# Performance work log

Measured on AMD Instinct MI355X. Metric: run time of the kernel, lower is better.

Reference implementation:

```python
import jax, jax.numpy as jnp
import numpy as np

B, NQ, NK = 4, 512, 512
DQ, DK, DV = 512, 512, 512
H = 128
MASK_VAL = -1e6


def setup_inputs() -> dict:
    key = jax.random.key(0)
    kq, kk, kv, kwq, kwk, kwv, kl = jax.random.split(key, 7)
    queries = jax.random.normal(kq, (B, NQ, DQ), dtype=jnp.float32)
    keys = jax.random.normal(kk, (B, NK, DK), dtype=jnp.float32)
    values = jax.random.normal(kv, (B, NK, DV), dtype=jnp.float32)
    # Dense(num_hiddens, use_bias=False) weights, Glorot-ish scale
    Wq = jax.random.normal(kwq, (DQ, H), dtype=jnp.float32) / np.sqrt(DQ)
    Wk = jax.random.normal(kwk, (DK, H), dtype=jnp.float32) / np.sqrt(DK)
    Wv = jax.random.normal(kwv, (H,), dtype=jnp.float32) / np.sqrt(H)  # Dense(1) as a vector
    valid_lens = jax.random.randint(kl, (B,), 1, NK + 1, dtype=jnp.int32)
    return {"queries": queries, "keys": keys, "values": values,
            "Wq": Wq, "Wk": Wk, "Wv": Wv, "valid_lens": valid_lens}


def reference(queries, keys, values, Wq, Wk, Wv, valid_lens):
    # Project queries/keys to hidden dim
    q = jnp.einsum('bqd,dh->bqh', queries, Wq)   # [B,NQ,H]
    k = jnp.einsum('bkd,dh->bkh', keys, Wk)      # [B,NK,H]
    # Broadcast add + tanh -> [B,NQ,NK,H] (the big intermediate)
    features = jnp.tanh(q[:, :, None, :] + k[:, None, :, :])
    # W_v reduces hidden dim to a scalar score
    scores = jnp.einsum('bqkh,h->bqk', features, Wv)  # [B,NQ,NK]
    # masked softmax over keys: positions >= valid_len get -1e6 (as in d2l sequence_mask)
    mask = jnp.arange(NK, dtype=jnp.int32)[None, None, :] < valid_lens[:, None, None]
    scores = jnp.where(mask, scores, MASK_VAL)
    attn = jax.nn.softmax(scores, axis=-1)
    # dropout rate 0.0 -> identity
    return jnp.einsum('bqk,bkv->bqv', attn, values)  # [B,NQ,DV]
```

## Files before the change

kernel.cpp:

```cpp
#include <hip/hip_runtime.h>

#ifndef __has_builtin
#define __has_builtin(x) 0
#endif

#if __has_builtin(__builtin_amdgcn_exp2f)
#define EXP2F(x) __builtin_amdgcn_exp2f(x)
#else
#define EXP2F(x) exp2f(x)
#endif
#if __has_builtin(__builtin_amdgcn_rcpf)
#define RCPF(x) __builtin_amdgcn_rcpf(x)
#else
#define RCPF(x) (1.0f / (x))
#endif

static constexpr int NB = 4, NQ = 512, NK = 512, DD = 512, HH = 128, DV = 512;
static constexpr float MASKV = -1e6f;
static constexpr float C2LOG2E = 2.885390081777926814f;

typedef __attribute__((ext_vector_type(8))) short bf16x8;
typedef __attribute__((ext_vector_type(4))) float f32x4;

__device__ __forceinline__ unsigned short f2bf(float x) {
  unsigned int u = __float_as_uint(x);
  u += 0x7FFFu + ((u >> 16) & 1u);
  return (unsigned short)(u >> 16);
}

__global__ __launch_bounds__(256) void proj_gemm_kernel(
    const float* __restrict__ queries, const float* __restrict__ keys,
    const float* __restrict__ Wq, const float* __restrict__ Wk,
    const int* __restrict__ valid_lens, float* __restrict__ projpart) {
  const int mt = blockIdx.x >> 3;
  const int ks = blockIdx.x & 7;
  const int row0 = mt << 6;
  const int k0 = ks << 6;
  const float* inb;
  const float* W;
  if (row0 >= 2048) {
    const int local = row0 - 2048;
    if ((local & 511) >= valid_lens[local >> 9]) return;
    inb = keys + (size_t)local * DD;
    W = Wk;
  } else {
    inb = queries + (size_t)row0 * DD;
    W = Wq;
  }

  __shared__ float aS[64][65];
  __shared__ __align__(16) float bS[64][128];

  const int t = threadIdx.x;
#pragma unroll
  for (int f = 0; f < 4; ++f) {
    const int idx = t + (f << 8);
    const int r = idx >> 4, d0 = (idx & 15) << 2;
    const float4 v = *reinterpret_cast<const float4*>(inb + (size_t)r * DD + k0 + d0);
    aS[r][d0] = v.x; aS[r][d0 + 1] = v.y; aS[r][d0 + 2] = v.z; aS[r][d0 + 3] = v.w;
  }
#pragma unroll
  for (int f = 0; f < 8; ++f) {
    const int idx = t + (f << 8);
    const int dk = idx >> 5, c4 = (idx & 31) << 2;
    *reinterpret_cast<float4*>(&bS[dk][c4]) =
        *reinterpret_cast<const float4*>(W + (size_t)(k0 + dk) * HH + c4);
  }
  __syncthreads();

  const int tv = t & 15, tr = t >> 4;
  float acc[4][8];
#pragma unroll
  for (int i = 0; i < 4; ++i)
#pragma unroll
    for (int j = 0; j < 8; ++j) acc[i][j] = 0.f;

#pragma unroll 8
  for (int dk = 0; dk < 64; ++dk) {
    const float av[4] = {aS[(tr << 2) + 0][dk], aS[(tr << 2) + 1][dk],
                         aS[(tr << 2) + 2][dk], aS[(tr << 2) + 3][dk]};
    const float4 b0 = *reinterpret_cast<const float4*>(&bS[dk][tv << 2]);
    const float4 b1 = *reinterpret_cast<const float4*>(&bS[dk][64 + (tv << 2)]);
    const float bv[8] = {b0.x, b0.y, b0.z, b0.w, b1.x, b1.y, b1.z, b1.w};
#pragma unroll
    for (int i = 0; i < 4; ++i)
#pragma unroll
      for (int j = 0; j < 8; ++j) acc[i][j] = fmaf(av[i], bv[j], acc[i][j]);
  }

  float* pb = projpart + ((size_t)ks << 19) + (size_t)row0 * HH;
#pragma unroll
  for (int i = 0; i < 4; ++i) {
    float* rowp = pb + (size_t)((tr << 2) + i) * HH;
    *reinterpret_cast<float4*>(rowp + (tv << 2)) =
        make_float4(acc[i][0], acc[i][1], acc[i][2], acc[i][3]);
    *reinterpret_cast<float4*>(rowp + 64 + (tv << 2)) =
        make_float4(acc[i][4], acc[i][5], acc[i][6], acc[i][7]);
  }
}

__global__ __launch_bounds__(256) void combo_kernel(
    const float* __restrict__ projpart, const float* __restrict__ values,
    const int* __restrict__ valid_lens,
    float* __restrict__ eq, float* __restrict__ ekT4,
    unsigned short* __restrict__ Vt) {
  const int bid = blockIdx.x;
  const int t = threadIdx.x;
  __shared__ unsigned short tl[64][72];

  if (bid < 256) {
    const float4* p = reinterpret_cast<const float4*>(projpart);
    const int i = bid * 256 + t;
    float4 s = p[i];
#pragma unroll
    for (int j = 1; j < 8; ++j) {
      const float4 v = p[i + j * 131072];
      s.x += v.x; s.y += v.y; s.z += v.z; s.w += v.w;
    }
    float4 r;
    r.x = EXP2F(s.x * C2LOG2E);
    r.y = EXP2F(s.y * C2LOG2E);
    r.z = EXP2F(s.z * C2LOG2E);
    r.w = EXP2F(s.w * C2LOG2E);
    reinterpret_cast<float4*>(eq)[i] = r;
  } else if (bid < 512) {
    const float4* p = reinterpret_cast<const float4*>(projpart);
    const int j = (bid - 256) * 256 + t;
    const int rl = j >> 5;
    const int b = rl >> 9, k = rl & 511;
    if (k >= valid_lens[b]) return;
    const int h4 = j & 31;
    float4 s = p[65536 + j];
#pragma unroll
    for (int jj = 1; jj < 8; ++jj) {
      const float4 v = p[65536 + j + jj * 131072];
      s.x += v.x; s.y += v.y; s.z += v.z; s.w += v.w;
    }
    float4 r;
    r.x = EXP2F(s.x * C2LOG2E);
    r.y = EXP2F(s.y * C2LOG2E);
    r.z = EXP2F(s.z * C2LOG2E);
    r.w = EXP2F(s.w * C2LOG2E);
    *reinterpret_cast<float4*>(ekT4 + ((((size_t)b * 32 + h4) << 9) + k) * 4) = r;
  } else {
    const int vb = bid - 512;
    const int b = vb >> 6;
    const int tile = vb & 63;
    const int k0 = (tile >> 3) << 6;
    const int v0 = (tile & 7) << 6;
    const int kr = t >> 4, c4 = (t & 15) << 2;
#pragma unroll
    for (int pp = 0; pp < 4; ++pp) {
      const int k = kr + (pp << 4);
      const float4 v = *reinterpret_cast<const float4*>(
          values + ((size_t)(b * NK + k0 + k)) * DV + v0 + c4);
      tl[k][c4 + 0] = f2bf(v.x); tl[k][c4 + 1] = f2bf(v.y);
      tl[k][c4 + 2] = f2bf(v.z); tl[k][c4 + 3] = f2bf(v.w);
    }
    __syncthreads();
    const int vr = t >> 2, seg = t & 3;
    unsigned int pk[8];
#pragma unroll
    for (int i = 0; i < 8; ++i) {
      const int kc = (seg << 4) + (i << 1);
      pk[i] = (unsigned int)tl[kc][vr] | ((unsigned int)tl[kc + 1][vr] << 16);
    }
    unsigned short* dst = Vt + ((size_t)(b * NK + v0 + vr)) * NK + k0 + (seg << 4);
    *reinterpret_cast<uint4*>(dst) = make_uint4(pk[0], pk[1], pk[2], pk[3]);
    *reinterpret_cast<uint4*>(dst + 8) = make_uint4(pk[4], pk[5], pk[6], pk[7]);
  }
}

__global__ __launch_bounds__(1024) void scores_softmax_kernel(
    const float* __restrict__ eq, const float* __restrict__ ekT4,
    const float* __restrict__ Wv, const int* __restrict__ valid_lens,
    unsigned short* __restrict__ attnQ) {
  const int b = blockIdx.x >> 7;
  const int q0 = (blockIdx.x & 127) << 2;
  const int t = threadIdx.x;
  const int kk = t & 511, hh = t >> 9;

  __shared__ __align__(16) float qs[4][HH];
  __shared__ __align__(16) float wv[HH];
  __shared__ __align__(16) float scp[2][4][NK];

  if (t < 512) {
    qs[t >> 7][t & 127] = eq[((size_t)(b * NQ + q0 + (t >> 7))) * HH + (t & 127)];
  } else if (t < 640) {
    wv[t - 512] = Wv[t - 512];
  }
  __syncthreads();

  const int vl = valid_lens[b];
  float s0 = 0.f, s1 = 0.f, s2 = 0.f, s3 = 0.f;

  if (kk < vl) {
    const float* ekb4 = ekT4 + (((size_t)(b * 32 + hh * 16) << 9) + kk) * 4;
#pragma unroll 8
    for (int i = 0; i < 16; ++i) {
      const float4 e4 = *reinterpret_cast<const float4*>(ekb4 + ((size_t)i << 11));
      const int h = (hh * 16 + i) << 2;
      const float4 w4 = *reinterpret_cast<const float4*>(&wv[h]);
      const float4 qa = *reinterpret_cast<const float4*>(&qs[0][h]);
      const float4 qb = *reinterpret_cast<const float4*>(&qs[1][h]);
      const float4 qc = *reinterpret_cast<const float4*>(&qs[2][h]);
      const float4 qd = *reinterpret_cast<const float4*>(&qs[3][h]);
      float d, r;
      d = fmaf(qa.x, e4.x, 1.f); r = RCPF(d); s0 = fmaf(w4.x, r, s0);
      d = fmaf(qa.y, e4.y, 1.f); r = RCPF(d); s0 = fmaf(w4.y, r, s0);
      d = fmaf(qa.z, e4.z, 1.f); r = RCPF(d); s0 = fmaf(w4.z, r, s0);
      d = fmaf(qa.w, e4.w, 1.f); r = RCPF(d); s0 = fmaf(w4.w, r, s0);
      d = fmaf(qb.x, e4.x, 1.f); r = RCPF(d); s1 = fmaf(w4.x, r, s1);
      d = fmaf(qb.y, e4.y, 1.f); r = RCPF(d); s1 = fmaf(w4.y, r, s1);
      d = fmaf(qb.z, e4.z, 1.f); r = RCPF(d); s1 = fmaf(w4.z, r, s1);
      d = fmaf(qb.w, e4.w, 1.f); r = RCPF(d); s1 = fmaf(w4.w, r, s1);
      d = fmaf(qc.x, e4.x, 1.f); r = RCPF(d); s2 = fmaf(w4.x, r, s2);
      d = fmaf(qc.y, e4.y, 1.f); r = RCPF(d); s2 = fmaf(w4.y, r, s2);
      d = fmaf(qc.z, e4.z, 1.f); r = RCPF(d); s2 = fmaf(w4.z, r, s2);
      d = fmaf(qc.w, e4.w, 1.f); r = RCPF(d); s2 = fmaf(w4.w, r, s2);
      d = fmaf(qd.x, e4.x, 1.f); r = RCPF(d); s3 = fmaf(w4.x, r, s3);
      d = fmaf(qd.y, e4.y, 1.f); r = RCPF(d); s3 = fmaf(w4.y, r, s3);
      d = fmaf(qd.z, e4.z, 1.f); r = RCPF(d); s3 = fmaf(w4.z, r, s3);
      d = fmaf(qd.w, e4.w, 1.f); r = RCPF(d); s3 = fmaf(w4.w, r, s3);
    }
  }
  scp[hh][0][kk] = s0;
  scp[hh][1][kk] = s1;
  scp[hh][2][kk] = s2;
  scp[hh][3][kk] = s3;
  __syncthreads();

  if (t < 256) {
    const int w = t >> 6, l = t & 63;
    float v[8];
#pragma unroll
    for (int j = 0; j < 8; ++j) {
      const int k = l + (j << 6);
      const float sv = scp[0][w][k] + scp[1][w][k];
      v[j] = (k < vl) ? (-2.f * sv) : MASKV;
    }
    float m = v[0];
#pragma unroll
    for (int j = 1; j < 8; ++j) m = fmaxf(m, v[j]);
#pragma unroll
    for (int off = 32; off > 0; off >>= 1) m = fmaxf(m, __shfl_xor(m, off, 64));
    float p[8], sum = 0.f;
#pragma unroll
    for (int j = 0; j < 8; ++j) {
      p[j] = __expf(v[j] - m);
      sum += p[j];
    }
#pragma unroll
    for (int off = 32; off > 0; off >>= 1) sum += __shfl_xor(sum, off, 64);
    const float inv = RCPF(sum);
#pragma unroll
    for (int j = 0; j < 8; ++j) scp[0][w][l + (j << 6)] = p[j] * inv;
  }
  __syncthreads();

  if (t < 512) {
#pragma unroll
    for (int j = 0; j < 4; ++j)
      attnQ[((size_t)(b * NQ + q0 + j)) * NK + t] = f2bf(scp[0][j][t]);
  }
}

__global__ __launch_bounds__(256) void pv_mfma_kernel(
    const unsigned short* __restrict__ attnQ, const unsigned short* __restrict__ Vt,
    const int* __restrict__ valid_lens, float* __restrict__ out) {
  const int bid = blockIdx.x;
  const int b = bid & 3;
  const int tile = bid >> 2;
  const int q0 = (tile >> 3) << 6;
  const int v0 = (tile & 7) << 6;

  __shared__ __align__(16) unsigned short Als[64 * 72];
  __shared__ __align__(16) unsigned short Bls[64 * 72];

  const int t = threadIdx.x;
  const int w = t >> 6, l = t & 63;
  const int wq = w >> 1, wv = w & 1;
  const int lm = l & 15;
  const int lk = (l >> 4) << 3;

  const f32x4 z = {0.f, 0.f, 0.f, 0.f};
  f32x4 acc[2][2] = {{z, z}, {z, z}};

  const int vl = valid_lens[b];
  const int nkt = (vl + 31) >> 5;

  const int sq = t >> 2, seg = t & 3;
  const unsigned short* arow = attnQ + ((size_t)(b * NQ + q0 + sq)) * NK;
  const unsigned short* brow = Vt + ((size_t)(b * NK + v0 + sq)) * NK;
  unsigned short* alds = &Als[sq * 72 + (seg << 3)];
  unsigned short* blds = &Bls[sq * 72 + (seg << 3)];

  for (int kt = 0; kt < nkt; ++kt) {
    const int k0 = kt << 5;
    *reinterpret_cast<bf16x8*>(alds) =
        *reinterpret_cast<const bf16x8*>(arow + k0 + (seg << 3));
    *reinterpret_cast<bf16x8*>(blds) =
        *reinterpret_cast<const bf16x8*>(brow + k0 + (seg << 3));
    __syncthreads();

    bf16x8 af[2], bfr[2];
#pragma unroll
    for (int mq = 0; mq < 2; ++mq)
      af[mq] = *reinterpret_cast<const bf16x8*>(
          &Als[(wq * 32 + mq * 16 + lm) * 72 + lk]);
#pragma unroll
    for (int nv = 0; nv < 2; ++nv)
      bfr[nv] = *reinterpret_cast<const bf16x8*>(
          &Bls[(wv * 32 + nv * 16 + lm) * 72 + lk]);
#pragma unroll
    for (int mq = 0; mq < 2; ++mq)
#pragma unroll
      for (int nv = 0; nv < 2; ++nv)
        acc[mq][nv] = __builtin_amdgcn_mfma_f32_16x16x32_bf16(
            af[mq], bfr[nv], acc[mq][nv], 0, 0, 0);
    __syncthreads();
  }

  const int rbase = (l >> 4) << 2;
#pragma unroll
  for (int mq = 0; mq < 2; ++mq) {
#pragma unroll
    for (int nv = 0; nv < 2; ++nv) {
      const int qg = q0 + wq * 32 + mq * 16 + rbase;
      const int vg = v0 + wv * 32 + nv * 16 + lm;
#pragma unroll
      for (int j = 0; j < 4; ++j)
        out[((size_t)(b * NQ + qg + j)) * DV + vg] = acc[mq][nv][j];
    }
  }
}

extern "C" void kernel_launch(void* const* d_in, const int* in_sizes, int n_in,
                              void* d_out, int out_size, void* d_ws, size_t ws_size,
                              hipStream_t stream) {
  (void)in_sizes; (void)n_in; (void)out_size; (void)ws_size;
  const float* queries = (const float*)d_in[0];
  const float* keys    = (const float*)d_in[1];
  const float* values  = (const float*)d_in[2];
  const float* Wq      = (const float*)d_in[3];
  const float* Wk      = (const float*)d_in[4];
  const float* Wv      = (const float*)d_in[5];
  const int*   vlens   = (const int*)d_in[6];
  float* out = (float*)d_out;
  float* ws = (float*)d_ws;

  float* eq   = ws;
  float* ekT4 = ws + 262144;
  unsigned short* attnQ = (unsigned short*)(ws + 524288);
  unsigned short* Vt    = (unsigned short*)(ws + 1048576);
  float* projpart = ws + 1572864;

  proj_gemm_kernel<<<512, 256, 0, stream>>>(queries, keys, Wq, Wk, vlens, projpart);
  combo_kernel<<<768, 256, 0, stream>>>(projpart, values, vlens, eq, ekT4, Vt);
  scores_softmax_kernel<<<512, 1024, 0, stream>>>(eq, ekT4, Wv, vlens, attnQ);
  pv_mfma_kernel<<<256, 256, 0, stream>>>(attnQ, Vt, vlens, out);
}
```

Measured before the change: 46.83 us.

## Enlarge projection GEMM tiles, move V transpose into projection kernel, drop LDS staging

After: 58.15 us. 24.2% more time.

```diff
diff --git a/kernel.cpp b/kernel.cpp
--- a/kernel.cpp
+++ b/kernel.cpp
@@ -28,88 +28,122 @@
   return (unsigned short)(u >> 16);
 }
 
-__global__ __launch_bounds__(256) void proj_gemm_kernel(
+__global__ __launch_bounds__(256) void proj_vt_kernel(
     const float* __restrict__ queries, const float* __restrict__ keys,
     const float* __restrict__ Wq, const float* __restrict__ Wk,
-    const int* __restrict__ valid_lens, float* __restrict__ projpart) {
-  const int mt = blockIdx.x >> 3;
-  const int ks = blockIdx.x & 7;
-  const int row0 = mt << 6;
-  const int k0 = ks << 6;
-  const float* inb;
-  const float* W;
-  if (row0 >= 2048) {
-    const int local = row0 - 2048;
-    if ((local & 511) >= valid_lens[local >> 9]) return;
-    inb = keys + (size_t)local * DD;
-    W = Wk;
-  } else {
-    inb = queries + (size_t)row0 * DD;
-    W = Wq;
-  }
-
-  __shared__ float aS[64][65];
-  __shared__ __align__(16) float bS[64][128];
-
-  const int t = threadIdx.x;
-#pragma unroll
-  for (int f = 0; f < 4; ++f) {
-    const int idx = t + (f << 8);
-    const int r = idx >> 4, d0 = (idx & 15) << 2;
-    const float4 v = *reinterpret_cast<const float4*>(inb + (size_t)r * DD + k0 + d0);
-    aS[r][d0] = v.x; aS[r][d0 + 1] = v.y; aS[r][d0 + 2] = v.z; aS[r][d0 + 3] = v.w;
-  }
-#pragma unroll
-  for (int f = 0; f < 8; ++f) {
-    const int idx = t + (f << 8);
-    const int dk = idx >> 5, c4 = (idx & 31) << 2;
-    *reinterpret_cast<float4*>(&bS[dk][c4]) =
-        *reinterpret_cast<const float4*>(W + (size_t)(k0 + dk) * HH + c4);
-  }
-  __syncthreads();
-
-  const int tv = t & 15, tr = t >> 4;
-  float acc[4][8];
-#pragma unroll
-  for (int i = 0; i < 4; ++i)
-#pragma unroll
-    for (int j = 0; j < 8; ++j) acc[i][j] = 0.f;
-
-#pragma unroll 8
-  for (int dk = 0; dk < 64; ++dk) {
-    const float av[4] = {aS[(tr << 2) + 0][dk], aS[(tr << 2) + 1][dk],
-                         aS[(tr << 2) + 2][dk], aS[(tr << 2) + 3][dk]};
-    const float4 b0 = *reinterpret_cast<const float4*>(&bS[dk][tv << 2]);
-    const float4 b1 = *reinterpret_cast<const float4*>(&bS[dk][64 + (tv << 2)]);
-    const float bv[8] = {b0.x, b0.y, b0.z, b0.w, b1.x, b1.y, b1.z, b1.w};
-#pragma unroll
-    for (int i = 0; i < 4; ++i)
-#pragma unroll
-      for (int j = 0; j < 8; ++j) acc[i][j] = fmaf(av[i], bv[j], acc[i][j]);
-  }
-
-  float* pb = projpart + ((size_t)ks << 19) + (size_t)row0 * HH;
-#pragma unroll
-  for (int i = 0; i < 4; ++i) {
-    float* rowp = pb + (size_t)((tr << 2) + i) * HH;
-    *reinterpret_cast<float4*>(rowp + (tv << 2)) =
-        make_float4(acc[i][0], acc[i][1], acc[i][2], acc[i][3]);
-    *reinterpret_cast<float4*>(rowp + 64 + (tv << 2)) =
-        make_float4(acc[i][4], acc[i][5], acc[i][6], acc[i][7]);
-  }
-}
-
-__global__ __launch_bounds__(256) void combo_kernel(
-    const float* __restrict__ projpart, const float* __restrict__ values,
-    const int* __restrict__ valid_lens,
-    float* __restrict__ eq, float* __restrict__ ekT4,
-    unsigned short* __restrict__ Vt) {
+    const float* __restrict__ values, const int* __restrict__ valid_lens,
+    float* __restrict__ projpart, unsigned short* __restrict__ Vt) {
+  __shared__ __align__(16) char smem[65536];
   const int bid = blockIdx.x;
   const int t = threadIdx.x;
-  __shared__ unsigned short tl[64][72];
 
   if (bid < 256) {
-    const float4* p = reinterpret_cast<const float4*>(projpart);
+    const int mt = bid >> 3;
+    const int ks = bid & 7;
+    const int row0 = mt << 7;
+    const int k0 = ks << 6;
+    const float* inb;
+    const float* W;
+    if (row0 >= 2048) {
+      const int local = row0 - 2048;
+      if ((local & 511) >= valid_lens[local >> 9]) return;
+      inb = keys + (size_t)local * DD;
+      W = Wk;
+    } else {
+      inb = queries + (size_t)row0 * DD;
+      W = Wq;
+    }
+    float* aT = reinterpret_cast<float*>(smem);
+    float* Wt = reinterpret_cast<float*>(smem + 32768);
+
+#pragma unroll
+    for (int f = 0; f < 8; ++f) {
+      const int idx = t + (f << 8);
+      const int r = idx & 127;
+      const int c4 = (idx >> 7) << 2;
+      const float4 v = *reinterpret_cast<const float4*>(inb + (size_t)r * DD + k0 + c4);
+      aT[(c4 + 0) * 128 + r] = v.x;
+      aT[(c4 + 1) * 128 + r] = v.y;
+      aT[(c4 + 2) * 128 + r] = v.z;
+      aT[(c4 + 3) * 128 + r] = v.w;
+    }
+#pragma unroll
+    for (int f = 0; f < 8; ++f) {
+      const int idx = t + (f << 8);
+      const int dk = idx >> 5, c4 = (idx & 31) << 2;
+      *reinterpret_cast<float4*>(Wt + dk * 128 + c4) =
+          *reinterpret_cast<const float4*>(W + (size_t)(k0 + dk) * HH + c4);
+    }
+    __syncthreads();
+
+    const int hg = t & 15;
+    const int rg = t >> 4;
+    float acc[8][8];
+#pragma unroll
+    for (int i = 0; i < 8; ++i)
+#pragma unroll
+      for (int j = 0; j < 8; ++j) acc[i][j] = 0.f;
+
+#pragma unroll 8
+    for (int dk = 0; dk < 64; ++dk) {
+      const float4 a0 = *reinterpret_cast<const float4*>(aT + dk * 128 + (rg << 3));
+      const float4 a1 = *reinterpret_cast<const float4*>(aT + dk * 128 + (rg << 3) + 4);
+      const float4 b0 = *reinterpret_cast<const float4*>(Wt + dk * 128 + (hg << 3));
+      const float4 b1 = *reinterpret_cast<const float4*>(Wt + dk * 128 + (hg << 3) + 4);
+      const float av[8] = {a0.x, a0.y, a0.z, a0.w, a1.x, a1.y, a1.z, a1.w};
+      const float bv[8] = {b0.x, b0.y, b0.z, b0.w, b1.x, b1.y, b1.z, b1.w};
+#pragma unroll
+      for (int i = 0; i < 8; ++i)
+#pragma unroll
+        for (int j = 0; j < 8; ++j) acc[i][j] = fmaf(av[i], bv[j], acc[i][j]);
+    }
+
+    float* pb = projpart + ((size_t)ks << 19) + (size_t)row0 * HH;
+#pragma unroll
+    for (int i = 0; i < 8; ++i) {
+      float* rowp = pb + (size_t)((rg << 3) + i) * HH + (hg << 3);
+      *reinterpret_cast<float4*>(rowp) =
+          make_float4(acc[i][0], acc[i][1], acc[i][2], acc[i][3]);
+      *reinterpret_cast<float4*>(rowp + 4) =
+          make_float4(acc[i][4], acc[i][5], acc[i][6], acc[i][7]);
+    }
+  } else {
+    unsigned short (*tl)[72] = reinterpret_cast<unsigned short (*)[72]>(smem);
+    const int vb = bid - 256;
+    const int b = vb >> 6;
+    const int tile = vb & 63;
+    const int k0 = (tile >> 3) << 6;
+    const int v0 = (tile & 7) << 6;
+    const int kr = t >> 4, c4 = (t & 15) << 2;
+#pragma unroll
+    for (int pp = 0; pp < 4; ++pp) {
+      const int k = kr + (pp << 4);
+      const float4 v = *reinterpret_cast<const float4*>(
+          values + ((size_t)(b * NK + k0 + k)) * DV + v0 + c4);
+      tl[k][c4 + 0] = f2bf(v.x); tl[k][c4 + 1] = f2bf(v.y);
+      tl[k][c4 + 2] = f2bf(v.z); tl[k][c4 + 3] = f2bf(v.w);
+    }
+    __syncthreads();
+    const int vr = t >> 2, seg = t & 3;
+    unsigned int pk[8];
+#pragma unroll
+    for (int i = 0; i < 8; ++i) {
+      const int kc = (seg << 4) + (i << 1);
+      pk[i] = (unsigned int)tl[kc][vr] | ((unsigned int)tl[kc + 1][vr] << 16);
+    }
+    unsigned short* dst = Vt + ((size_t)(b * NK + v0 + vr)) * NK + k0 + (seg << 4);
+    *reinterpret_cast<uint4*>(dst) = make_uint4(pk[0], pk[1], pk[2], pk[3]);
+    *reinterpret_cast<uint4*>(dst + 8) = make_uint4(pk[4], pk[5], pk[6], pk[7]);
+  }
+}
+
+__global__ __launch_bounds__(256) void reduce_kernel(
+    const float* __restrict__ projpart, const int* __restrict__ valid_lens,
+    float* __restrict__ eq, float* __restrict__ ekT4) {
+  const int bid = blockIdx.x;
+  const int t = threadIdx.x;
+  const float4* p = reinterpret_cast<const float4*>(projpart);
+  if (bid < 256) {
     const int i = bid * 256 + t;
     float4 s = p[i];
 #pragma unroll
@@ -123,8 +157,7 @@
     r.z = EXP2F(s.z * C2LOG2E);
     r.w = EXP2F(s.w * C2LOG2E);
     reinterpret_cast<float4*>(eq)[i] = r;
-  } else if (bid < 512) {
-    const float4* p = reinterpret_cast<const float4*>(projpart);
+  } else {
     const int j = (bid - 256) * 256 + t;
     const int rl = j >> 5;
     const int b = rl >> 9, k = rl & 511;
@@ -142,32 +175,6 @@
     r.z = EXP2F(s.z * C2LOG2E);
     r.w = EXP2F(s.w * C2LOG2E);
     *reinterpret_cast<float4*>(ekT4 + ((((size_t)b * 32 + h4) << 9) + k) * 4) = r;
-  } else {
-    const int vb = bid - 512;
-    const int b = vb >> 6;
-    const int tile = vb & 63;
-    const int k0 = (tile >> 3) << 6;
-    const int v0 = (tile & 7) << 6;
-    const int kr = t >> 4, c4 = (t & 15) << 2;
-#pragma unroll
-    for (int pp = 0; pp < 4; ++pp) {
-      const int k = kr + (pp << 4);
-      const float4 v = *reinterpret_cast<const float4*>(
-          values + ((size_t)(b * NK + k0 + k)) * DV + v0 + c4);
-      tl[k][c4 + 0] = f2bf(v.x); tl[k][c4 + 1] = f2bf(v.y);
-      tl[k][c4 + 2] = f2bf(v.z); tl[k][c4 + 3] = f2bf(v.w);
-    }
-    __syncthreads();
-    const int vr = t >> 2, seg = t & 3;
-    unsigned int pk[8];
-#pragma unroll
-    for (int i = 0; i < 8; ++i) {
-      const int kc = (seg << 4) + (i << 1);
-      pk[i] = (unsigned int)tl[kc][vr] | ((unsigned int)tl[kc + 1][vr] << 16);
-    }
-    unsigned short* dst = Vt + ((size_t)(b * NK + v0 + vr)) * NK + k0 + (seg << 4);
-    *reinterpret_cast<uint4*>(dst) = make_uint4(pk[0], pk[1], pk[2], pk[3]);
-    *reinterpret_cast<uint4*>(dst + 8) = make_uint4(pk[4], pk[5], pk[6], pk[7]);
   }
 }
 
@@ -180,31 +187,26 @@
   const int t = threadIdx.x;
   const int kk = t & 511, hh = t >> 9;
 
-  __shared__ __align__(16) float qs[4][HH];
-  __shared__ __align__(16) float wv[HH];
   __shared__ __align__(16) float scp[2][4][NK];
-
-  if (t < 512) {
-    qs[t >> 7][t & 127] = eq[((size_t)(b * NQ + q0 + (t >> 7))) * HH + (t & 127)];
-  } else if (t < 640) {
-    wv[t - 512] = Wv[t - 512];
-  }
-  __syncthreads();
 
   const int vl = valid_lens[b];
   float s0 = 0.f, s1 = 0.f, s2 = 0.f, s3 = 0.f;
 
   if (kk < vl) {
     const float* ekb4 = ekT4 + (((size_t)(b * 32 + hh * 16) << 9) + kk) * 4;
-#pragma unroll 8
+    const float* qrow0 = eq + ((size_t)(b * NQ + q0 + 0)) * HH;
+    const float* qrow1 = eq + ((size_t)(b * NQ + q0 + 1)) * HH;
+    const float* qrow2 = eq + ((size_t)(b * NQ + q0 + 2)) * HH;
+    const float* qrow3 = eq + ((size_t)(b * NQ + q0 + 3)) * HH;
+#pragma unroll 4
     for (int i = 0; i < 16; ++i) {
       const float4 e4 = *reinterpret_cast<const float4*>(ekb4 + ((size_t)i << 11));
       const int h = (hh * 16 + i) << 2;
-      const float4 w4 = *reinterpret_cast<const float4*>(&wv[h]);
-      const float4 qa = *reinterpret_cast<const float4*>(&qs[0][h]);
-      const float4 qb = *reinterpret_cast<const float4*>(&qs[1][h]);
-      const float4 qc = *reinterpret_cast<const float4*>(&qs[2][h]);
-      const float4 qd = *reinterpret_cast<const float4*>(&qs[3][h]);
+      const float4 w4 = *reinterpret_cast<const float4*>(Wv + h);
+      const float4 qa = *reinterpret_cast<const float4*>(qrow0 + h);
+      const float4 qb = *reinterpret_cast<const float4*>(qrow1 + h);
+      const float4 qc = *reinterpret_cast<const float4*>(qrow2 + h);
+      const float4 qd = *reinterpret_cast<const float4*>(qrow3 + h);
       float d, r;
       d = fmaf(qa.x, e4.x, 1.f); r = RCPF(d); s0 = fmaf(w4.x, r, s0);
       d = fmaf(qa.y, e4.y, 1.f); r = RCPF(d); s0 = fmaf(w4.y, r, s0);
@@ -355,8 +357,9 @@
   unsigned short* Vt    = (unsigned short*)(ws + 1048576);
   float* projpart = ws + 1572864;
 
-  proj_gemm_kernel<<<512, 256, 0, stream>>>(queries, keys, Wq, Wk, vlens, projpart);
-  combo_kernel<<<768, 256, 0, stream>>>(projpart, values, vlens, eq, ekT4, Vt);
+  proj_vt_kernel<<<512, 256, 0, stream>>>(queries, keys, Wq, Wk, values, vlens,
+                                          projpart, Vt);
+  reduce_kernel<<<512, 256, 0, stream>>>(projpart, vlens, eq, ekT4);
   scores_softmax_kernel<<<512, 1024, 0, stream>>>(eq, ekT4, Wv, vlens, attnQ);
   pv_mfma_kernel<<<256, 256, 0, stream>>>(attnQ, Vt, vlens, out);
 }
```

## Fuse projection GEMM with exp and V transpose using split-bf16 MFMA

Applied to the files above, without the earlier changes.

New measurement: 42.06 us. 1.11x faster.

```diff
diff --git a/kernel.cpp b/kernel.cpp
--- a/kernel.cpp
+++ b/kernel.cpp
@@ -27,123 +27,143 @@
   u += 0x7FFFu + ((u >> 16) & 1u);
   return (unsigned short)(u >> 16);
 }
-
-__global__ __launch_bounds__(256) void proj_gemm_kernel(
+__device__ __forceinline__ float bf2f(unsigned short h) {
+  return __uint_as_float(((unsigned int)h) << 16);
+}
+__device__ __forceinline__ void split2(float x, unsigned short& hi, unsigned short& lo) {
+  hi = f2bf(x);
+  lo = f2bf(x - bf2f(hi));
+}
+
+__global__ __launch_bounds__(256) void proj_mfma_vt_kernel(
     const float* __restrict__ queries, const float* __restrict__ keys,
     const float* __restrict__ Wq, const float* __restrict__ Wk,
-    const int* __restrict__ valid_lens, float* __restrict__ projpart) {
-  const int mt = blockIdx.x >> 3;
-  const int ks = blockIdx.x & 7;
-  const int row0 = mt << 6;
-  const int k0 = ks << 6;
-  const float* inb;
-  const float* W;
-  if (row0 >= 2048) {
-    const int local = row0 - 2048;
-    if ((local & 511) >= valid_lens[local >> 9]) return;
-    inb = keys + (size_t)local * DD;
-    W = Wk;
-  } else {
-    inb = queries + (size_t)row0 * DD;
-    W = Wq;
-  }
-
-  __shared__ float aS[64][65];
-  __shared__ __align__(16) float bS[64][128];
-
-  const int t = threadIdx.x;
-#pragma unroll
-  for (int f = 0; f < 4; ++f) {
-    const int idx = t + (f << 8);
-    const int r = idx >> 4, d0 = (idx & 15) << 2;
-    const float4 v = *reinterpret_cast<const float4*>(inb + (size_t)r * DD + k0 + d0);
-    aS[r][d0] = v.x; aS[r][d0 + 1] = v.y; aS[r][d0 + 2] = v.z; aS[r][d0 + 3] = v.w;
-  }
-#pragma unroll
-  for (int f = 0; f < 8; ++f) {
-    const int idx = t + (f << 8);
-    const int dk = idx >> 5, c4 = (idx & 31) << 2;
-    *reinterpret_cast<float4*>(&bS[dk][c4]) =
-        *reinterpret_cast<const float4*>(W + (size_t)(k0 + dk) * HH + c4);
-  }
-  __syncthreads();
-
-  const int tv = t & 15, tr = t >> 4;
-  float acc[4][8];
-#pragma unroll
-  for (int i = 0; i < 4; ++i)
-#pragma unroll
-    for (int j = 0; j < 8; ++j) acc[i][j] = 0.f;
-
-#pragma unroll 8
-  for (int dk = 0; dk < 64; ++dk) {
-    const float av[4] = {aS[(tr << 2) + 0][dk], aS[(tr << 2) + 1][dk],
-                         aS[(tr << 2) + 2][dk], aS[(tr << 2) + 3][dk]};
-    const float4 b0 = *reinterpret_cast<const float4*>(&bS[dk][tv << 2]);
-    const float4 b1 = *reinterpret_cast<const float4*>(&bS[dk][64 + (tv << 2)]);
-    const float bv[8] = {b0.x, b0.y, b0.z, b0.w, b1.x, b1.y, b1.z, b1.w};
-#pragma unroll
-    for (int i = 0; i < 4; ++i)
-#pragma unroll
-      for (int j = 0; j < 8; ++j) acc[i][j] = fmaf(av[i], bv[j], acc[i][j]);
-  }
-
-  float* pb = projpart + ((size_t)ks << 19) + (size_t)row0 * HH;
-#pragma unroll
-  for (int i = 0; i < 4; ++i) {
-    float* rowp = pb + (size_t)((tr << 2) + i) * HH;
-    *reinterpret_cast<float4*>(rowp + (tv << 2)) =
-        make_float4(acc[i][0], acc[i][1], acc[i][2], acc[i][3]);
-    *reinterpret_cast<float4*>(rowp + 64 + (tv << 2)) =
-        make_float4(acc[i][4], acc[i][5], acc[i][6], acc[i][7]);
-  }
-}
-
-__global__ __launch_bounds__(256) void combo_kernel(
-    const float* __restrict__ projpart, const float* __restrict__ values,
-    const int* __restrict__ valid_lens,
+    const float* __restrict__ values, const int* __restrict__ valid_lens,
     float* __restrict__ eq, float* __restrict__ ekT4,
     unsigned short* __restrict__ Vt) {
+  __shared__ __align__(16) unsigned short smem_us[20736];
   const int bid = blockIdx.x;
   const int t = threadIdx.x;
-  __shared__ unsigned short tl[64][72];
 
   if (bid < 256) {
-    const float4* p = reinterpret_cast<const float4*>(projpart);
-    const int i = bid * 256 + t;
-    float4 s = p[i];
-#pragma unroll
-    for (int j = 1; j < 8; ++j) {
-      const float4 v = p[i + j * 131072];
-      s.x += v.x; s.y += v.y; s.z += v.z; s.w += v.w;
-    }
-    float4 r;
-    r.x = EXP2F(s.x * C2LOG2E);
-    r.y = EXP2F(s.y * C2LOG2E);
-    r.z = EXP2F(s.z * C2LOG2E);
-    r.w = EXP2F(s.w * C2LOG2E);
-    reinterpret_cast<float4*>(eq)[i] = r;
-  } else if (bid < 512) {
-    const float4* p = reinterpret_cast<const float4*>(projpart);
-    const int j = (bid - 256) * 256 + t;
-    const int rl = j >> 5;
-    const int b = rl >> 9, k = rl & 511;
-    if (k >= valid_lens[b]) return;
-    const int h4 = j & 31;
-    float4 s = p[65536 + j];
-#pragma unroll
-    for (int jj = 1; jj < 8; ++jj) {
-      const float4 v = p[65536 + j + jj * 131072];
-      s.x += v.x; s.y += v.y; s.z += v.z; s.w += v.w;
-    }
-    float4 r;
-    r.x = EXP2F(s.x * C2LOG2E);
-    r.y = EXP2F(s.y * C2LOG2E);
-    r.z = EXP2F(s.z * C2LOG2E);
-    r.w = EXP2F(s.w * C2LOG2E);
-    *reinterpret_cast<float4*>(ekT4 + ((((size_t)b * 32 + h4) << 9) + k) * 4) = r;
+    const int row0 = bid << 4;
+    const bool isK = row0 >= 2048;
+    int b = 0, kloc = 0;
+    const float* inb;
+    const float* W;
+    if (isK) {
+      const int local = row0 - 2048;
+      b = local >> 9;
+      kloc = local & 511;
+      if (kloc >= valid_lens[b]) return;
+      inb = keys + (size_t)local * DD;
+      W = Wk;
+    } else {
+      inb = queries + (size_t)row0 * DD;
+      W = Wq;
+    }
+
+    unsigned short* Ah = smem_us;
+    unsigned short* Al = smem_us + 1152;
+    unsigned short* Wh = smem_us + 2304;
+    unsigned short* Wl = smem_us + 11520;
+
+    const int w = t >> 6, l = t & 63;
+    const int lm = l & 15;
+    const int lk8 = (l >> 4) << 3;
+
+    const f32x4 z = {0.f, 0.f, 0.f, 0.f};
+    f32x4 acc[2] = {z, z};
+
+    const int ar = t >> 4, ac4 = (t & 15) << 2;
+    const int wh = t & 127, wkg = (t >> 7) << 5;
+
+    for (int kt = 0; kt < 8; ++kt) {
+      const int k0 = kt << 6;
+      {
+        const float4 v = *reinterpret_cast<const float4*>(inb + (size_t)ar * DD + k0 + ac4);
+        unsigned short h0, h1, h2, h3, l0, l1, l2, l3;
+        split2(v.x, h0, l0); split2(v.y, h1, l1);
+        split2(v.z, h2, l2); split2(v.w, h3, l3);
+        uint2 ph = make_uint2((unsigned int)h0 | ((unsigned int)h1 << 16),
+                              (unsigned int)h2 | ((unsigned int)h3 << 16));
+        uint2 pl = make_uint2((unsigned int)l0 | ((unsigned int)l1 << 16),
+                              (unsigned int)l2 | ((unsigned int)l3 << 16));
+        *reinterpret_cast<uint2*>(Ah + ar * 72 + ac4) = ph;
+        *reinterpret_cast<uint2*>(Al + ar * 72 + ac4) = pl;
+      }
+      {
+        unsigned int hw[16], lw[16];
+#pragma unroll
+        for (int i = 0; i < 16; ++i) {
+          const float w0 = W[(size_t)(k0 + wkg + 2 * i) * HH + wh];
+          const float w1 = W[(size_t)(k0 + wkg + 2 * i + 1) * HH + wh];
+          unsigned short a0, a1, b0, b1;
+          split2(w0, a0, b0); split2(w1, a1, b1);
+          hw[i] = (unsigned int)a0 | ((unsigned int)a1 << 16);
+          lw[i] = (unsigned int)b0 | ((unsigned int)b1 << 16);
+        }
+        unsigned int* dh = reinterpret_cast<unsigned int*>(Wh + wh * 72 + wkg);
+        unsigned int* dl = reinterpret_cast<unsigned int*>(Wl + wh * 72 + wkg);
+#pragma unroll
+        for (int i = 0; i < 4; ++i) {
+          *reinterpret_cast<uint4*>(dh + 4 * i) =
+              make_uint4(hw[4 * i], hw[4 * i + 1], hw[4 * i + 2], hw[4 * i + 3]);
+          *reinterpret_cast<uint4*>(dl + 4 * i) =
+              make_uint4(lw[4 * i], lw[4 * i + 1], lw[4 * i + 2], lw[4 * i + 3]);
+        }
+      }
+      __syncthreads();
+
+#pragma unroll
+      for (int kh = 0; kh < 2; ++kh) {
+        const int ko = lk8 + (kh << 5);
+        const bf16x8 ah = *reinterpret_cast<const bf16x8*>(Ah + lm * 72 + ko);
+        const bf16x8 al = *reinterpret_cast<const bf16x8*>(Al + lm * 72 + ko);
+#pragma unroll
+        for (int c = 0; c < 2; ++c) {
+          const int hrow = (w << 5) + (c << 4) + lm;
+          const bf16x8 bh = *reinterpret_cast<const bf16x8*>(Wh + hrow * 72 + ko);
+          const bf16x8 bl = *reinterpret_cast<const bf16x8*>(Wl + hrow * 72 + ko);
+          acc[c] = __builtin_amdgcn_mfma_f32_16x16x32_bf16(ah, bh, acc[c], 0, 0, 0);
+          acc[c] = __builtin_amdgcn_mfma_f32_16x16x32_bf16(al, bh, acc[c], 0, 0, 0);
+          acc[c] = __builtin_amdgcn_mfma_f32_16x16x32_bf16(ah, bl, acc[c], 0, 0, 0);
+        }
+      }
+      __syncthreads();
+    }
+
+    const int rb = (l >> 4) << 2;
+    if (!isK) {
+#pragma unroll
+      for (int c = 0; c < 2; ++c) {
+        const int h = (w << 5) + (c << 4) + lm;
+#pragma unroll
+        for (int j = 0; j < 4; ++j)
+          eq[(size_t)(row0 + rb + j) * HH + h] = EXP2F(acc[c][j] * C2LOG2E);
+      }
+    } else {
+      float* tile = reinterpret_cast<float*>(smem_us);
+#pragma unroll
+      for (int c = 0; c < 2; ++c) {
+        const int h = (w << 5) + (c << 4) + lm;
+#pragma unroll
+        for (int j = 0; j < 4; ++j)
+          tile[(rb + j) * 132 + h] = EXP2F(acc[c][j] * C2LOG2E);
+      }
+      __syncthreads();
+#pragma unroll
+      for (int i = 0; i < 2; ++i) {
+        const int idx = t + (i << 8);
+        const int k = idx & 15, h4 = idx >> 4;
+        const float4 v = *reinterpret_cast<const float4*>(tile + k * 132 + (h4 << 2));
+        *reinterpret_cast<float4*>(
+            ekT4 + ((((size_t)b * 32 + h4) << 9) + kloc + k) * 4) = v;
+      }
+    }
   } else {
-    const int vb = bid - 512;
+    unsigned short (*tl)[72] = reinterpret_cast<unsigned short (*)[72]>(smem_us);
+    const int vb = bid - 256;
     const int b = vb >> 6;
     const int tile = vb & 63;
     const int k0 = (tile >> 3) << 6;
@@ -353,10 +373,9 @@
   float* ekT4 = ws + 262144;
   unsigned short* attnQ = (unsigned short*)(ws + 524288);
   unsigned short* Vt    = (unsigned short*)(ws + 1048576);
-  float* projpart = ws + 1572864;
-
-  proj_gemm_kernel<<<512, 256, 0, stream>>>(queries, keys, Wq, Wk, vlens, projpart);
-  combo_kernel<<<768, 256, 0, stream>>>(projpart, values, vlens, eq, ekT4, Vt);
+
+  proj_mfma_vt_kernel<<<512, 256, 0, stream>>>(queries, keys, Wq, Wk, values,
+                                               vlens, eq, ekT4, Vt);
   scores_softmax_kernel<<<512, 1024, 0, stream>>>(eq, ekT4, Wv, vlens, attnQ);
   pv_mfma_kernel<<<256, 256, 0, stream>>>(attnQ, Vt, vlens, out);
 }
```
